# Performance work log

Hardware: AMD Instinct MI355X
Metric: run time of the kernel (lower is better)

## Reference

```python
import jax, jax.numpy as jnp
import numpy as np

HEAD_SIZE = 64

def setup_inputs() -> dict:
    key = jax.random.key(0)
    k1, k2, k3, k4 = jax.random.split(key, 4)
    B, T, C = 4, 4096, 1024
    x = jax.random.normal(k1, (B, T, C), dtype=jnp.float32)
    scale = 1.0 / np.sqrt(C)
    Wk = jax.random.normal(k2, (C, HEAD_SIZE), dtype=jnp.float32) * scale
    Wq = jax.random.normal(k3, (C, HEAD_SIZE), dtype=jnp.float32) * scale
    Wv = jax.random.normal(k4, (C, HEAD_SIZE), dtype=jnp.float32) * scale
    return {"x": x, "Wk": Wk, "Wq": Wq, "Wv": Wv}

def reference(x, Wk, Wq, Wv):
    B, T, C = x.shape
    k = jnp.einsum('btc,ch->bth', x, Wk)   # [B,T,H]
    q = jnp.einsum('btc,ch->bth', x, Wq)
    v = jnp.einsum('btc,ch->bth', x, Wv)
    # Faithful to the source: scores = k @ q^T (NOT the usual q @ k^T)
    wei = jnp.einsum('bth,bsh->bts', k, q) * (HEAD_SIZE ** -0.5)  # [B,T,T]
    causal = jnp.tril(jnp.ones((T, T), dtype=bool))
    wei = jnp.where(causal, wei, -jnp.inf)
    wei = jax.nn.softmax(wei, axis=-1)
    # dropout_rate = 0.0 -> identity
    out = jnp.einsum('bts,bsh->bth', wei, v)  # [B,T,H]
    return out
```

## Files before the change

kernel.cpp:

```cpp
#include <hip/hip_runtime.h>


typedef __attribute__((ext_vector_type(8))) short short8;
typedef __attribute__((ext_vector_type(4))) short s16x4;
typedef __attribute__((ext_vector_type(4))) float f32x4;
typedef unsigned short u16;

#define MFMA16(A, B, C) __builtin_amdgcn_mfma_f32_16x16x32_bf16((A), (B), (C), 0, 0, 0)

__device__ __forceinline__ u16 f2b(float f) {
    __bf16 h = (__bf16)f;
    return __builtin_bit_cast(u16, h);
}
__device__ __forceinline__ float b2f(u16 v) {
    return __builtin_bit_cast(float, (unsigned int)v << 16);
}

__device__ __forceinline__ void gload16(const void* g, void* l) {
    __builtin_amdgcn_global_load_lds(
        (const __attribute__((address_space(1))) unsigned int*)g,
        (__attribute__((address_space(3))) unsigned int*)l, 16, 0, 0);
}

__global__ __launch_bounds__(256) void wt_kernel(const float* __restrict__ Wk,
                                                 const float* __restrict__ Wq,
                                                 const float* __restrict__ Wv,
                                                 u16* __restrict__ WtF) {
    const int kc = blockIdx.x;
    const int mat = blockIdx.y;
    const float* W = (mat == 0) ? Wk : (mat == 1 ? Wq : Wv);
    const int tid = threadIdx.x;
    const int tl = tid >> 6, lane = tid & 63, quad = lane >> 4, l16 = lane & 15;
    short8 v;
#pragma unroll
    for (int j = 0; j < 8; ++j)
        v[j] = f2b(W[(size_t)(kc * 32 + quad * 8 + j) * 64 + tl * 16 + l16]);
    const size_t dst = ((size_t)((mat * 4 + tl) * 32 + kc) * 64 + lane) * 8;
#pragma unroll
    for (int rep = 0; rep < 8; ++rep)
        *(short8*)(WtF + (size_t)rep * 196608 + dst) = v;
}

__global__ __launch_bounds__(256) void proj_kernel(const float* __restrict__ x,
                                                   const u16* __restrict__ WtF,
                                                   u16* __restrict__ Kb,
                                                   u16* __restrict__ Qb,
                                                   u16* __restrict__ Vt) {
    __shared__ char smem[65536];
    const int tid = threadIdx.x;
    const int w = tid >> 6, lane = tid & 63, quad = lane >> 4, l16 = lane & 15;
    const int mbase = blockIdx.x * 32;
    const u16* Wrep = WtF + (size_t)(blockIdx.x & 7) * 196608;
    const char* xblk = (const char*)x + (size_t)mbase * 4096;
    const int wbase16 = (w << 6) * 16;

    f32x4 acc[2][3];
#pragma unroll
    for (int r = 0; r < 2; ++r)
#pragma unroll
        for (int c = 0; c < 3; ++c) acc[r][c] = (f32x4)(0.0f);

#define STAGE(buf, p) do {                                                          \
        char* la = smem + (buf) * 8192;                                             \
        char* lb = smem + 16384 + (buf) * 24576;                                    \
        _Pragma("unroll")                                                           \
        for (int i = 0; i < 2; ++i) {                                               \
            int u = i * 256 + tid;                                                  \
            int row = u >> 4;                                                       \
            int cb = ((u & 15) * 16) ^ ((row & 7) << 5);                            \
            gload16(xblk + (size_t)row * 4096 + (size_t)(p) * 256 + cb,             \
                    la + i * 4096 + wbase16);                                       \
        }                                                                           \
        _Pragma("unroll")                                                           \
        for (int i = 0; i < 6; ++i) {                                               \
            int u = i * 256 + tid;                                                  \
            gload16(Wrep + (size_t)(u >> 7) * 16384 + (size_t)(p) * 1024 + (u & 127) * 8, \
                    lb + i * 4096 + wbase16);                                       \
        }                                                                           \
    } while (0)

    STAGE(0, 0);
    __syncthreads();

    for (int t = 0; t < 16; ++t) {
        const int cur = t & 1;
        if (t < 15) STAGE(cur ^ 1, t + 1);
        const char* Ab = smem + cur * 8192;
        const char* Bb = smem + 16384 + cur * 24576;
#pragma unroll
        for (int kk = 0; kk < 2; ++kk) {
            short8 af[2];
#pragma unroll
            for (int r = 0; r < 2; ++r) {
                const int row = r * 16 + l16;
                const int c0 = (kk * 128 + quad * 32) ^ ((l16 & 7) << 5);
                f32x4 lo = *(const f32x4*)(Ab + row * 256 + c0);
                f32x4 hi = *(const f32x4*)(Ab + row * 256 + (c0 ^ 16));
                short8 a;
#pragma unroll
                for (int j = 0; j < 4; ++j) {
                    a[j]     = (short)f2b(lo[j]);
                    a[j + 4] = (short)f2b(hi[j]);
                }
                af[r] = a;
            }
#pragma unroll
            for (int c = 0; c < 3; ++c) {
                short8 bf = *(const short8*)(Bb + (((w * 3 + c) * 2 + kk) * 64 + lane) * 16);
                acc[0][c] = MFMA16(af[0], bf, acc[0][c]);
                acc[1][c] = MFMA16(af[1], bf, acc[1][c]);
            }
        }
        __syncthreads();
    }
#undef STAGE

    u16 (*tile)[200] = (u16(*)[200])smem;
#pragma unroll
    for (int r = 0; r < 2; ++r)
#pragma unroll
        for (int c = 0; c < 3; ++c)
#pragma unroll
            for (int reg = 0; reg < 4; ++reg)
                tile[r * 16 + quad * 4 + reg][(w * 3 + c) * 16 + l16] = f2b(acc[r][c][reg]);
    __syncthreads();

    const int b = mbase >> 12, t0b = mbase & 4095;
    {
        const int row = tid >> 3, cu8 = (tid & 7) * 8;
        short8 vk = *(const short8*)&tile[row][cu8];
        *(short8*)(Kb + (size_t)(mbase + row) * 64 + cu8) = vk;
        short8 vq = *(const short8*)&tile[row][64 + cu8];
#pragma unroll
        for (int r = 0; r < 4; ++r)
            *(short8*)(Qb + (size_t)r * 1048576 + (size_t)(mbase + row) * 64 + cu8) = vq;
    }
    {
        const int h = tid >> 2, toff = (tid & 3) * 8;
        short8 vv;
#pragma unroll
        for (int j = 0; j < 8; ++j) vv[j] = tile[toff + j][128 + h];
#pragma unroll
        for (int r = 0; r < 4; ++r)
            *(short8*)(Vt + (size_t)r * 1048576 + ((size_t)(b * 64 + h) << 12) + t0b + toff) = vv;
    }
}

#define QSWZ(row, cb) ((row) * 128 + ((cb) ^ (((row) & 7) << 4)))
#define VSWZ(row, cb) ((row) * 256 + ((cb) ^ (((row) & 15) << 4)))
__global__ __launch_bounds__(256) void attn_kernel(const u16* __restrict__ Kb,
                                                   const u16* __restrict__ Qb,
                                                   const u16* __restrict__ Vt,
                                                   u16* __restrict__ Op,
                                                   float* __restrict__ Ml) {
    const int pc = blockIdx.x;
    const int b = blockIdx.y;
    const int pair = pc / 5, c5 = pc - pair * 5;
    const int nLow = (pair >> 4) + 1;
    const int tile  = (c5 < nLow) ? pair : (63 - pair);
    const int chunk = (c5 < nLow) ? c5 : (c5 - nLow);
    __shared__ char smem[50176];
    const int tid = threadIdx.x;
    const int w = tid >> 6, lane = tid & 63, quad = lane >> 4, l16 = lane & 15;
    char* psB = smem + 32768 + w * 4352;
    const int t0 = tile * 64;
    const int bsBeg = chunk * 8;
    const int bsEnd = min(chunk * 8 + 7, tile >> 1);
    const int bsDiag = tile >> 1;

    const u16* Qp = Qb + (size_t)(tile & 3) * 1048576;
    const u16* Vp = Vt + (size_t)(tile & 3) * 1048576;

    int qd[4], vd[4];
    size_t qg[4], vg[4];
#pragma unroll
    for (int i = 0; i < 4; ++i) {
        const int lin = tid + i * 256;
        qd[i] = QSWZ(lin >> 3, (lin & 7) * 16);
        vd[i] = VSWZ(lin >> 4, (lin & 15) * 16);
        qg[i] = ((size_t)(b << 12) + (lin >> 3)) * 64 + (lin & 7) * 8;
        vg[i] = ((size_t)(b * 64 + (lin >> 4)) << 12) + (lin & 15) * 8;
    }

    short8 aK[2];
#pragma unroll
    for (int kk = 0; kk < 2; ++kk)
        aK[kk] = *(const short8*)(Kb + (size_t)((b << 12) + t0 + w * 16 + l16) * 64 + kk * 32 + quad * 8);

    short8 qr[4], vr[4];
#pragma unroll
    for (int i = 0; i < 4; ++i) {
        qr[i] = *(const short8*)(Qp + qg[i] + (size_t)bsBeg * 8192);
        vr[i] = *(const short8*)(Vp + vg[i] + bsBeg * 128);
    }

    float l_acc = 0.0f;
    f32x4 O[4];
#pragma unroll
    for (int ht = 0; ht < 4; ++ht) O[ht] = (f32x4)(0.0f);

    const int tg = t0 + w * 16 + l16;

    for (int bs = bsBeg; bs <= bsEnd; ++bs) {
        __syncthreads();
#pragma unroll
        for (int i = 0; i < 4; ++i) {
            *(short8*)(smem + qd[i]) = qr[i];
            *(short8*)(smem + 16384 + vd[i]) = vr[i];
        }
        __syncthreads();
        if (bs < bsEnd) {
#pragma unroll
            for (int i = 0; i < 4; ++i) {
                qr[i] = *(const short8*)(Qp + qg[i] + (size_t)(bs + 1) * 8192);
                vr[i] = *(const short8*)(Vp + vg[i] + (bs + 1) * 128);
            }
        }

        f32x4 sc[8];
#pragma unroll
        for (int nt = 0; nt < 8; ++nt) sc[nt] = (f32x4)(0.0f);
#pragma unroll
        for (int kk = 0; kk < 2; ++kk)
#pragma unroll
            for (int nt = 0; nt < 8; ++nt) {
                short8 aq = *(const short8*)(smem + QSWZ(nt * 16 + l16, kk * 64 + quad * 16));
                sc[nt] = MFMA16(aq, aK[kk], sc[nt]);
            }

#pragma unroll
        for (int nt = 0; nt < 8; ++nt) {
            const int sgBase = bs * 128 + nt * 16 + quad * 4;
            s16x4 v4;
#pragma unroll
            for (int reg = 0; reg < 4; ++reg) {
                float v = sc[nt][reg];
                if (bs == bsDiag && sgBase + reg > tg) v = -1e30f;
                float p = exp2f(v * 0.18033688011112042f);
                l_acc += p;
                v4[reg] = (short)f2b(p);
            }
            *(s16x4*)(psB + l16 * 272 + nt * 32 + quad * 8) = v4;
        }

#pragma unroll
        for (int kk = 0; kk < 4; ++kk) {
            short8 ap = *(const short8*)(psB + l16 * 272 + kk * 64 + quad * 16);
#pragma unroll
            for (int ht = 0; ht < 4; ++ht) {
                short8 bv = *(const short8*)(smem + 16384 + VSWZ(ht * 16 + l16, kk * 64 + quad * 16));
                O[ht] = MFMA16(ap, bv, O[ht]);
            }
        }
    }

    const int slot = ((b * 64 + tile) * 4 + chunk);
    {
        float v = l_acc;
        v += __shfl_xor(v, 16);
        v += __shfl_xor(v, 32);
        if (quad == 0) Ml[(size_t)slot * 64 + w * 16 + l16] = v;
    }
    const int trow = w * 16 + quad * 4;
#pragma unroll
    for (int ht = 0; ht < 4; ++ht)
#pragma unroll
        for (int reg = 0; reg < 4; ++reg)
            Op[(size_t)slot * 4096 + (size_t)(trow + reg) * 64 + ht * 16 + l16] = f2b(O[ht][reg]);
}

__global__ __launch_bounds__(256) void combine_kernel(const u16* __restrict__ Op,
                                                      const float* __restrict__ Ml,
                                                      float* __restrict__ out) {
    const int tid = threadIdx.x, cu = tid & 7, r0 = tid >> 3;
    const int tile = blockIdx.x, b = blockIdx.y;
    const int nch = tile / 16 + 1;
    const int slotBase = (b * 64 + tile) * 4;
#pragma unroll
    for (int i = 0; i < 2; ++i) {
        const int row = r0 + 32 * i;
        float L = 0.0f, acc[8];
#pragma unroll
        for (int j = 0; j < 8; ++j) acc[j] = 0.0f;
#pragma unroll
        for (int c = 0; c < 4; ++c) {
            const bool act = c < nch;
            float lraw = Ml[(size_t)(slotBase + c) * 64 + row];
            short8 ov = *(const short8*)(Op + (size_t)(slotBase + c) * 4096 + (size_t)row * 64 + cu * 8);
            L += act ? lraw : 0.0f;
#pragma unroll
            for (int j = 0; j < 8; ++j)
                acc[j] += act ? b2f((u16)ov[j]) : 0.0f;
        }
        float inv = 1.0f / L;
        float* dst = out + ((size_t)(b << 12) + tile * 64 + row) * 64 + cu * 8;
        *(float4*)(dst)     = make_float4(acc[0] * inv, acc[1] * inv, acc[2] * inv, acc[3] * inv);
        *(float4*)(dst + 4) = make_float4(acc[4] * inv, acc[5] * inv, acc[6] * inv, acc[7] * inv);
    }
}

extern "C" void kernel_launch(void* const* d_in, const int* in_sizes, int n_in,
                              void* d_out, int out_size, void* d_ws, size_t ws_size,
                              hipStream_t stream) {
    const float* x  = (const float*)d_in[0];
    const float* Wk = (const float*)d_in[1];
    const float* Wq = (const float*)d_in[2];
    const float* Wv = (const float*)d_in[3];

    u16* ws16 = (u16*)d_ws;
    u16* Wt = ws16;
    u16* Kb = Wt + 1572864;
    u16* Qb = Kb + 1048576;
    u16* Vt = Qb + 4194304;
    u16* Op = Vt + 4194304;
    float* Ml = (float*)(Op + 8388608);

    wt_kernel<<<dim3(32, 3), 256, 0, stream>>>(Wk, Wq, Wv, Wt);
    proj_kernel<<<512, 256, 0, stream>>>(x, Wt, Kb, Qb, Vt);
    attn_kernel<<<dim3(160, 4), 256, 0, stream>>>(Kb, Qb, Vt, Op, Ml);
    combine_kernel<<<dim3(64, 4), 256, 0, stream>>>(Op, Ml, (float*)d_out);
}
```

Before: 148.6 us.

## Fuse paired low/high query tiles into one block sharing staged Q/V chunks

Each attention block now handles both tile p and its mirror tile 63-p for the same key chunk. The Q/V data staged in shared memory is reused for two score and PV passes, which cuts global loads and block count from 160 to 112 per batch. In exchange each block holds two sets of accumulators, raising register pressure, and per-block work becomes less even. An unused TILE_PASS macro is left defined.

```diff
diff --git a/kernel.cpp b/kernel.cpp
--- a/kernel.cpp
+++ b/kernel.cpp
@@ -155,21 +155,22 @@
                                                    float* __restrict__ Ml) {
     const int pc = blockIdx.x;
     const int b = blockIdx.y;
-    const int pair = pc / 5, c5 = pc - pair * 5;
-    const int nLow = (pair >> 4) + 1;
-    const int tile  = (c5 < nLow) ? pair : (63 - pair);
-    const int chunk = (c5 < nLow) ? c5 : (c5 - nLow);
+    int p, c;
+    if (pc < 64) { p = pc >> 2; c = pc & 3; }
+    else { int i = pc - 64; p = 16 + i / 3; c = i - (p - 16) * 3; }
+    const int tLo = p, tHi = 63 - p;
+    const int nLow = (p >> 4) + 1;
+    const bool hasLo = (c < nLow);
     __shared__ char smem[50176];
     const int tid = threadIdx.x;
     const int w = tid >> 6, lane = tid & 63, quad = lane >> 4, l16 = lane & 15;
     char* psB = smem + 32768 + w * 4352;
-    const int t0 = tile * 64;
-    const int bsBeg = chunk * 8;
-    const int bsEnd = min(chunk * 8 + 7, tile >> 1);
-    const int bsDiag = tile >> 1;
-
-    const u16* Qp = Qb + (size_t)(tile & 3) * 1048576;
-    const u16* Vp = Vt + (size_t)(tile & 3) * 1048576;
+    const int bsBeg = c * 8;
+    const int bsDiagLo = tLo >> 1, bsDiagHi = tHi >> 1;
+    const int bsEnd = min(c * 8 + 7, bsDiagHi);
+
+    const u16* Qp = Qb + (size_t)(p & 3) * 1048576;
+    const u16* Vp = Vt + (size_t)(p & 3) * 1048576;
 
     int qd[4], vd[4];
     size_t qg[4], vg[4];
@@ -182,10 +183,12 @@
         vg[i] = ((size_t)(b * 64 + (lin >> 4)) << 12) + (lin & 15) * 8;
     }
 
-    short8 aK[2];
-#pragma unroll
-    for (int kk = 0; kk < 2; ++kk)
-        aK[kk] = *(const short8*)(Kb + (size_t)((b << 12) + t0 + w * 16 + l16) * 64 + kk * 32 + quad * 8);
+    short8 aKlo[2], aKhi[2];
+#pragma unroll
+    for (int kk = 0; kk < 2; ++kk) {
+        aKlo[kk] = *(const short8*)(Kb + (size_t)((b << 12) + tLo * 64 + w * 16 + l16) * 64 + kk * 32 + quad * 8);
+        aKhi[kk] = *(const short8*)(Kb + (size_t)((b << 12) + tHi * 64 + w * 16 + l16) * 64 + kk * 32 + quad * 8);
+    }
 
     short8 qr[4], vr[4];
 #pragma unroll
@@ -194,12 +197,13 @@
         vr[i] = *(const short8*)(Vp + vg[i] + bsBeg * 128);
     }
 
-    float l_acc = 0.0f;
-    f32x4 O[4];
-#pragma unroll
-    for (int ht = 0; ht < 4; ++ht) O[ht] = (f32x4)(0.0f);
-
-    const int tg = t0 + w * 16 + l16;
+    float lLo = 0.0f, lHi = 0.0f;
+    f32x4 Olo[4], Ohi[4];
+#pragma unroll
+    for (int ht = 0; ht < 4; ++ht) { Olo[ht] = (f32x4)(0.0f); Ohi[ht] = (f32x4)(0.0f); }
+
+    const int tgLo = tLo * 64 + w * 16 + l16;
+    const int tgHi = tHi * 64 + w * 16 + l16;
 
     for (int bs = bsBeg; bs <= bsEnd; ++bs) {
         __syncthreads();
@@ -216,57 +220,143 @@
                 vr[i] = *(const short8*)(Vp + vg[i] + (bs + 1) * 128);
             }
         }
-
-        f32x4 sc[8];
-#pragma unroll
-        for (int nt = 0; nt < 8; ++nt) sc[nt] = (f32x4)(0.0f);
-#pragma unroll
-        for (int kk = 0; kk < 2; ++kk)
+        const bool doLo = hasLo && (bs <= bsDiagLo);
+
+#define TILE_PASS(aK, diagBs, tg, l_acc, O)                                          \
+        do {                                                                         \
+            f32x4 sc[8];                                                             \
+            _Pragma("unroll")                                                        \
+            for (int nt = 0; nt < 8; ++nt) sc[nt] = (f32x4)(0.0f);                   \
+            _Pragma("unroll")                                                        \
+            for (int kk = 0; kk < 2; ++kk)                                           \
+                _Pragma("unroll")                                                    \
+                for (int nt = 0; nt < 8; ++nt) {                                     \
+                    short8 aq = *(const short8*)(smem + QSWZ(nt * 16 + l16, kk * 64 + quad * 16)); \
+                    sc[nt] = MFMA16(aq, (aK), sc[nt]);                               \
+                }                                                                    \
+            _Pragma("unroll")                                                        \
+            for (int nt = 0; nt < 8; ++nt) {                                         \
+                const int sgBase = bs * 128 + nt * 16 + quad * 4;                    \
+                s16x4 v4;                                                            \
+                _Pragma("unroll")                                                    \
+                for (int reg = 0; reg < 4; ++reg) {                                  \
+                    float v = sc[nt][reg];                                           \
+                    if (bs == (diagBs) && sgBase + reg > (tg)) v = -1e30f;           \
+                    float pp = exp2f(v * 0.18033688011112042f);                      \
+                    (l_acc) += pp;                                                   \
+                    v4[reg] = (short)f2b(pp);                                        \
+                }                                                                    \
+                *(s16x4*)(psB + l16 * 272 + nt * 32 + quad * 8) = v4;                \
+            }                                                                        \
+            _Pragma("unroll")                                                        \
+            for (int kk = 0; kk < 4; ++kk) {                                         \
+                short8 ap = *(const short8*)(psB + l16 * 272 + kk * 64 + quad * 16); \
+                _Pragma("unroll")                                                    \
+                for (int ht = 0; ht < 4; ++ht) {                                     \
+                    short8 bv = *(const short8*)(smem + 16384 + VSWZ(ht * 16 + l16, kk * 64 + quad * 16)); \
+                    (O)[ht] = MFMA16(ap, bv, (O)[ht]);                               \
+                }                                                                    \
+            }                                                                        \
+        } while (0)
+
+        {
+            f32x4 sc[8];
+#pragma unroll
+            for (int nt = 0; nt < 8; ++nt) sc[nt] = (f32x4)(0.0f);
+#pragma unroll
+            for (int kk = 0; kk < 2; ++kk)
+#pragma unroll
+                for (int nt = 0; nt < 8; ++nt) {
+                    short8 aq = *(const short8*)(smem + QSWZ(nt * 16 + l16, kk * 64 + quad * 16));
+                    sc[nt] = MFMA16(aq, aKhi[kk], sc[nt]);
+                }
 #pragma unroll
             for (int nt = 0; nt < 8; ++nt) {
-                short8 aq = *(const short8*)(smem + QSWZ(nt * 16 + l16, kk * 64 + quad * 16));
-                sc[nt] = MFMA16(aq, aK[kk], sc[nt]);
-            }
-
-#pragma unroll
-        for (int nt = 0; nt < 8; ++nt) {
-            const int sgBase = bs * 128 + nt * 16 + quad * 4;
-            s16x4 v4;
-#pragma unroll
-            for (int reg = 0; reg < 4; ++reg) {
-                float v = sc[nt][reg];
-                if (bs == bsDiag && sgBase + reg > tg) v = -1e30f;
-                float p = exp2f(v * 0.18033688011112042f);
-                l_acc += p;
-                v4[reg] = (short)f2b(p);
-            }
-            *(s16x4*)(psB + l16 * 272 + nt * 32 + quad * 8) = v4;
-        }
-
-#pragma unroll
-        for (int kk = 0; kk < 4; ++kk) {
-            short8 ap = *(const short8*)(psB + l16 * 272 + kk * 64 + quad * 16);
-#pragma unroll
-            for (int ht = 0; ht < 4; ++ht) {
-                short8 bv = *(const short8*)(smem + 16384 + VSWZ(ht * 16 + l16, kk * 64 + quad * 16));
-                O[ht] = MFMA16(ap, bv, O[ht]);
-            }
-        }
-    }
-
-    const int slot = ((b * 64 + tile) * 4 + chunk);
+                const int sgBase = bs * 128 + nt * 16 + quad * 4;
+                s16x4 v4;
+#pragma unroll
+                for (int reg = 0; reg < 4; ++reg) {
+                    float v = sc[nt][reg];
+                    if (bs == bsDiagHi && sgBase + reg > tgHi) v = -1e30f;
+                    float pp = exp2f(v * 0.18033688011112042f);
+                    lHi += pp;
+                    v4[reg] = (short)f2b(pp);
+                }
+                *(s16x4*)(psB + l16 * 272 + nt * 32 + quad * 8) = v4;
+            }
+#pragma unroll
+            for (int kk = 0; kk < 4; ++kk) {
+                short8 ap = *(const short8*)(psB + l16 * 272 + kk * 64 + quad * 16);
+#pragma unroll
+                for (int ht = 0; ht < 4; ++ht) {
+                    short8 bv = *(const short8*)(smem + 16384 + VSWZ(ht * 16 + l16, kk * 64 + quad * 16));
+                    Ohi[ht] = MFMA16(ap, bv, Ohi[ht]);
+                }
+            }
+        }
+        if (doLo) {
+            f32x4 sc[8];
+#pragma unroll
+            for (int nt = 0; nt < 8; ++nt) sc[nt] = (f32x4)(0.0f);
+#pragma unroll
+            for (int kk = 0; kk < 2; ++kk)
+#pragma unroll
+                for (int nt = 0; nt < 8; ++nt) {
+                    short8 aq = *(const short8*)(smem + QSWZ(nt * 16 + l16, kk * 64 + quad * 16));
+                    sc[nt] = MFMA16(aq, aKlo[kk], sc[nt]);
+                }
+#pragma unroll
+            for (int nt = 0; nt < 8; ++nt) {
+                const int sgBase = bs * 128 + nt * 16 + quad * 4;
+                s16x4 v4;
+#pragma unroll
+                for (int reg = 0; reg < 4; ++reg) {
+                    float v = sc[nt][reg];
+                    if (bs == bsDiagLo && sgBase + reg > tgLo) v = -1e30f;
+                    float pp = exp2f(v * 0.18033688011112042f);
+                    lLo += pp;
+                    v4[reg] = (short)f2b(pp);
+                }
+                *(s16x4*)(psB + l16 * 272 + nt * 32 + quad * 8) = v4;
+            }
+#pragma unroll
+            for (int kk = 0; kk < 4; ++kk) {
+                short8 ap = *(const short8*)(psB + l16 * 272 + kk * 64 + quad * 16);
+#pragma unroll
+                for (int ht = 0; ht < 4; ++ht) {
+                    short8 bv = *(const short8*)(smem + 16384 + VSWZ(ht * 16 + l16, kk * 64 + quad * 16));
+                    Olo[ht] = MFMA16(ap, bv, Olo[ht]);
+                }
+            }
+        }
+#undef TILE_PASS
+    }
+
+    const int trow = w * 16 + quad * 4;
     {
-        float v = l_acc;
+        const int slot = ((b * 64 + tHi) * 4 + c);
+        float v = lHi;
         v += __shfl_xor(v, 16);
         v += __shfl_xor(v, 32);
         if (quad == 0) Ml[(size_t)slot * 64 + w * 16 + l16] = v;
-    }
-    const int trow = w * 16 + quad * 4;
-#pragma unroll
-    for (int ht = 0; ht < 4; ++ht)
-#pragma unroll
-        for (int reg = 0; reg < 4; ++reg)
-            Op[(size_t)slot * 4096 + (size_t)(trow + reg) * 64 + ht * 16 + l16] = f2b(O[ht][reg]);
+#pragma unroll
+        for (int ht = 0; ht < 4; ++ht)
+#pragma unroll
+            for (int reg = 0; reg < 4; ++reg)
+                Op[(size_t)slot * 4096 + (size_t)(trow + reg) * 64 + ht * 16 + l16] = f2b(Ohi[ht][reg]);
+    }
+    if (hasLo) {
+        const int slot = ((b * 64 + tLo) * 4 + c);
+        float v = lLo;
+        v += __shfl_xor(v, 16);
+        v += __shfl_xor(v, 32);
+        if (quad == 0) Ml[(size_t)slot * 64 + w * 16 + l16] = v;
+#pragma unroll
+        for (int ht = 0; ht < 4; ++ht)
+#pragma unroll
+            for (int reg = 0; reg < 4; ++reg)
+                Op[(size_t)slot * 4096 + (size_t)(trow + reg) * 64 + ht * 16 + l16] = f2b(Olo[ht][reg]);
+    }
 }
 
 __global__ __launch_bounds__(256) void combine_kernel(const u16* __restrict__ Op,
@@ -317,6 +407,6 @@
 
     wt_kernel<<<dim3(32, 3), 256, 0, stream>>>(Wk, Wq, Wv, Wt);
     proj_kernel<<<512, 256, 0, stream>>>(x, Wt, Kb, Qb, Vt);
-    attn_kernel<<<dim3(160, 4), 256, 0, stream>>>(Kb, Qb, Vt, Op, Ml);
+    attn_kernel<<<dim3(112, 4), 256, 0, stream>>>(Kb, Qb, Vt, Op, Ml);
     combine_kernel<<<dim3(64, 4), 256, 0, stream>>>(Op, Ml, (float*)d_out);
 }
```

Result: slower. 158.1 us (+6.4%).
